# Kernel optimization log

Measured on AMD Instinct MI355X. Metric: run time of the kernel, lower is better.

## Reference

```python
import jax, jax.numpy as jnp
import numpy as np

HIDDEN = 512

def flip_sequences(x, lengths):
    # flax sst2-style flip: reverse each sequence's first `length` items, padding stays at end
    B, T = x.shape[0], x.shape[1]
    idxs = (jnp.arange(T - 1, -1, -1)[None, :] + lengths[:, None]) % T  # [B,T]
    return x[jnp.arange(B)[:, None], idxs]

def lstm_scan(x, Wi, Wh, b):
    # x: [B,T,D] -> outputs [B,T,H]; flax OptimizedLSTMCell math (gate order i,f,g,o)
    B = x.shape[0]
    H = Wh.shape[0]
    xW = jnp.einsum('btd,dg->tbg', x, Wi) + b  # precompute input projections, time-major [T,B,4H]
    def step(carry, xw):
        c, h = carry
        gates = xw + h @ Wh
        i, f, g, o = jnp.split(gates, 4, axis=-1)
        c = jax.nn.sigmoid(f) * c + jax.nn.sigmoid(i) * jnp.tanh(g)
        h = jax.nn.sigmoid(o) * jnp.tanh(c)
        return (c, h), h
    init = (jnp.zeros((B, H), x.dtype), jnp.zeros((B, H), x.dtype))
    _, hs = jax.lax.scan(step, init, xW)  # hs: [T,B,H]
    return jnp.swapaxes(hs, 0, 1)

def setup_inputs() -> dict:
    key = jax.random.key(0)
    ks = jax.random.split(key, 8)
    B, T, D, H = 16, 2048, 512, HIDDEN
    s_in = 1.0 / np.sqrt(D)
    s_h = 1.0 / np.sqrt(H)
    return {
        'inputs': jax.random.normal(ks[0], (B, T, D), jnp.float32),
        'lengths': jax.random.randint(ks[1], (B,), 1, T + 1, jnp.int32),
        'Wi_f': jax.random.normal(ks[2], (D, 4 * H), jnp.float32) * s_in,
        'Wh_f': jax.random.normal(ks[3], (H, 4 * H), jnp.float32) * s_h,
        'b_f': jnp.zeros((4 * H,), jnp.float32),
        'Wi_b': jax.random.normal(ks[4], (D, 4 * H), jnp.float32) * s_in,
        'Wh_b': jax.random.normal(ks[5], (H, 4 * H), jnp.float32) * s_h,
        'b_b': jnp.zeros((4 * H,), jnp.float32),
    }

def reference(inputs, lengths, Wi_f, Wh_f, b_f, Wi_b, Wh_b, b_b):
    fwd = lstm_scan(inputs, Wi_f, Wh_f, b_f)  # [B,T,H]
    rev_in = flip_sequences(inputs, lengths)
    bwd = lstm_scan(rev_in, Wi_b, Wh_b, b_b)
    bwd = flip_sequences(bwd, lengths)
    return jnp.concatenate([fwd, bwd], axis=-1)  # [B,T,2H]
```

## Files before the change

### kernel.cpp

```cpp
#include <hip/hip_runtime.h>
#include <cstdint>
#include <cstddef>

#define T_SEQ 2048
#define BATCH 16
#define DIM   512
#define HID   512
#define KTOT  1024
#define NCOL  2048
#define APAD  8
#define AROW  (KTOT + APAD)

typedef __attribute__((ext_vector_type(8))) short          s8v;
typedef __attribute__((ext_vector_type(4))) float          f4v;
typedef __attribute__((ext_vector_type(4))) unsigned short h4v;

__device__ __forceinline__ unsigned short f2b(float f) {
  unsigned u = __builtin_bit_cast(unsigned, f);
  return (unsigned short)((u + 0x7fffu + ((u >> 16) & 1u)) >> 16);
}

__global__ __launch_bounds__(256, 1)
void lstm_persist(const float* __restrict__ x, const int* __restrict__ lengths,
                  const float* __restrict__ Wi_f, const float* __restrict__ Wh_f,
                  const float* __restrict__ b_f,
                  const float* __restrict__ Wi_b, const float* __restrict__ Wh_b,
                  const float* __restrict__ b_b,
                  unsigned int* __restrict__ flags,
                  float* __restrict__ out) {
  __shared__ unsigned short A[BATCH][AROW];
  __shared__ float glds[4][BATCH][16];

  const int w    = (int)blockIdx.x;
  const int dir  = w >> 5;
  const int g    = w & 31;
  const int j0   = g * 16;
  const int tid  = (int)threadIdx.x;
  const int lane = tid & 63;
  const int wv   = tid >> 6;
  const int b    = tid >> 4;
  const int sub  = tid & 15;
  const int len  = lengths[b];

  const float* bias = dir ? b_b : b_f;
  const float bi = bias[0 * HID + j0 + sub];
  const float bf = bias[1 * HID + j0 + sub];
  const float bg = bias[2 * HID + j0 + sub];
  const float bo = bias[3 * HID + j0 + sub];

  s8v wfrag[32];
  {
    const float* Wi = dir ? Wi_b : Wi_f;
    const float* Wh = dir ? Wh_b : Wh_f;
    const int col = wv * HID + j0 + (lane & 15);
    const int kb  = (lane >> 4) * 8;
#pragma unroll
    for (int kc = 0; kc < 16; ++kc) {
      const float* src = Wi + (size_t)(kc * 32 + kb) * NCOL + col;
      s8v f;
#pragma unroll
      for (int j = 0; j < 8; ++j) f[j] = (short)f2b(src[(size_t)j * NCOL]);
      wfrag[kc] = f;
    }
#pragma unroll
    for (int kc = 0; kc < 16; ++kc) {
      const float* src = Wh + (size_t)(kc * 32 + kb) * NCOL + col;
      s8v f;
#pragma unroll
      for (int j = 0; j < 8; ++j) f[j] = (short)f2b(src[(size_t)j * NCOL]);
      wfrag[16 + kc] = f;
    }
  }

  float c_state = 0.f;
  const int arow = lane & 15;
  const int koff = (lane >> 4) * 8;
  unsigned int* myflag = flags + (size_t)(dir * 32 + g) * 16;
  unsigned int* pollbase = flags + (size_t)(dir * 32) * 16;

  {
    const int tau0 = dir ? ((T_SEQ - 1 + len) & (T_SEQ - 1)) : 0;
    const float* xrow = x + ((size_t)b * T_SEQ + tau0) * DIM;
#pragma unroll
    for (int r = 0; r < 8; ++r) {
      const int k = sub * 4 + r * 64;
      f4v v = *(const f4v*)(xrow + k);
      h4v p; p[0] = f2b(v[0]); p[1] = f2b(v[1]); p[2] = f2b(v[2]); p[3] = f2b(v[3]);
      *(h4v*)&A[b][k] = p;
      h4v z = (h4v){0, 0, 0, 0};
      *(h4v*)&A[b][DIM + k] = z;
    }
  }
  __syncthreads();

  for (int t = 0; t < T_SEQ; ++t) {
    const int tau = dir ? ((T_SEQ - 1 - t + len) & (T_SEQ - 1)) : t;
    const bool notlast = (t + 1 < T_SEQ);

    f4v xv[8];
    if (notlast) {
      const int taun = dir ? ((T_SEQ - 2 - t + len) & (T_SEQ - 1)) : (t + 1);
      const float* xrow = x + ((size_t)b * T_SEQ + taun) * DIM;
#pragma unroll
      for (int r = 0; r < 8; ++r) xv[r] = *(const f4v*)(xrow + sub * 4 + r * 64);
    }

    f4v acc0 = {0.f,0.f,0.f,0.f}, acc1 = {0.f,0.f,0.f,0.f};
    f4v acc2 = {0.f,0.f,0.f,0.f}, acc3 = {0.f,0.f,0.f,0.f};
    {
      const unsigned short* ap = &A[arow][koff];
#pragma unroll
      for (int kc = 0; kc < 32; kc += 4) {
        s8v a0 = *(const s8v*)(ap + (kc + 0) * 32);
        s8v a1 = *(const s8v*)(ap + (kc + 1) * 32);
        s8v a2 = *(const s8v*)(ap + (kc + 2) * 32);
        s8v a3 = *(const s8v*)(ap + (kc + 3) * 32);
        acc0 = __builtin_amdgcn_mfma_f32_16x16x32_bf16(a0, wfrag[kc + 0], acc0, 0, 0, 0);
        acc1 = __builtin_amdgcn_mfma_f32_16x16x32_bf16(a1, wfrag[kc + 1], acc1, 0, 0, 0);
        acc2 = __builtin_amdgcn_mfma_f32_16x16x32_bf16(a2, wfrag[kc + 2], acc2, 0, 0, 0);
        acc3 = __builtin_amdgcn_mfma_f32_16x16x32_bf16(a3, wfrag[kc + 3], acc3, 0, 0, 0);
      }
    }
#pragma unroll
    for (int r = 0; r < 4; ++r)
      glds[wv][(lane >> 4) * 4 + r][lane & 15] = (acc0[r] + acc1[r]) + (acc2[r] + acc3[r]);
    __syncthreads();

    {
      const float gi = glds[0][b][sub] + bi;
      const float gf = glds[1][b][sub] + bf;
      const float gg = glds[2][b][sub] + bg;
      const float go = glds[3][b][sub] + bo;
      const float si = 1.f / (1.f + __expf(-gi));
      const float sf = 1.f / (1.f + __expf(-gf));
      const float so = 1.f / (1.f + __expf(-go));
      const float tg = 1.f - 2.f / (1.f + __expf(2.f * gg));
      c_state = sf * c_state + si * tg;
      const float tc = 1.f - 2.f / (1.f + __expf(2.f * c_state));
      const float h = so * tc;
      __hip_atomic_store(out + ((size_t)b * T_SEQ + tau) * (2 * HID) + (size_t)dir * HID + j0 + sub,
                         h, __ATOMIC_RELAXED, __HIP_MEMORY_SCOPE_AGENT);
    }

    if (notlast) {
#pragma unroll
      for (int r = 0; r < 8; ++r) {
        const int k = sub * 4 + r * 64;
        h4v p; p[0] = f2b(xv[r][0]); p[1] = f2b(xv[r][1]);
               p[2] = f2b(xv[r][2]); p[3] = f2b(xv[r][3]);
        *(h4v*)&A[b][k] = p;
      }

      asm volatile("s_waitcnt vmcnt(0)" ::: "memory");
      __syncthreads();
      if (tid == 0)
        __hip_atomic_store(myflag, (unsigned)(t + 1), __ATOMIC_RELAXED, __HIP_MEMORY_SCOPE_AGENT);
      {
        const unsigned tgt = (unsigned)(t + 1);
        while (true) {
          unsigned v = __hip_atomic_load(pollbase + (size_t)(lane & 31) * 16,
                                         __ATOMIC_RELAXED, __HIP_MEMORY_SCOPE_AGENT);
          if (__all(v >= tgt)) break;
          __builtin_amdgcn_s_sleep(1);
        }
      }

      const float* hrow = out + ((size_t)b * T_SEQ + tau) * (2 * HID) + (size_t)dir * HID;
      unsigned long long hu[16];
#pragma unroll
      for (int r = 0; r < 8; ++r) {
        const int k = sub * 4 + r * 64;
        hu[2 * r]     = __hip_atomic_load((const unsigned long long*)(hrow + k),
                                          __ATOMIC_RELAXED, __HIP_MEMORY_SCOPE_AGENT);
        hu[2 * r + 1] = __hip_atomic_load((const unsigned long long*)(hrow + k) + 1,
                                          __ATOMIC_RELAXED, __HIP_MEMORY_SCOPE_AGENT);
      }
#pragma unroll
      for (int r = 0; r < 8; ++r) {
        const int k = sub * 4 + r * 64;
        const float f0 = __builtin_bit_cast(float, (unsigned)(hu[2 * r] & 0xffffffffu));
        const float f1 = __builtin_bit_cast(float, (unsigned)(hu[2 * r] >> 32));
        const float f2 = __builtin_bit_cast(float, (unsigned)(hu[2 * r + 1] & 0xffffffffu));
        const float f3 = __builtin_bit_cast(float, (unsigned)(hu[2 * r + 1] >> 32));
        h4v p; p[0] = f2b(f0); p[1] = f2b(f1); p[2] = f2b(f2); p[3] = f2b(f3);
        *(h4v*)&A[b][DIM + k] = p;
      }
      __syncthreads();
    }
  }
}

extern "C" void kernel_launch(void* const* d_in, const int* in_sizes, int n_in,
                              void* d_out, int out_size, void* d_ws, size_t ws_size,
                              hipStream_t stream) {
  const float* x    = (const float*)d_in[0];
  const int*   len  = (const int*)d_in[1];
  const float* Wi_f = (const float*)d_in[2];
  const float* Wh_f = (const float*)d_in[3];
  const float* b_f  = (const float*)d_in[4];
  const float* Wi_b = (const float*)d_in[5];
  const float* Wh_b = (const float*)d_in[6];
  const float* b_b  = (const float*)d_in[7];
  float* out = (float*)d_out;
  unsigned int* flags = (unsigned int*)d_ws;

  hipMemsetAsync(d_ws, 0, 4096, stream);
  hipLaunchKernelGGL(lstm_persist, dim3(64), dim3(256), 0, stream,
                     x, len, Wi_f, Wh_f, b_f, Wi_b, Wh_b, b_b, flags, out);
}
```

Before: 6.430 ms.

## Replace flag barrier with step-tagged bf16 hidden-state exchange buffer

```diff
diff --git a/kernel.cpp b/kernel.cpp
--- a/kernel.cpp
+++ b/kernel.cpp
@@ -15,6 +15,8 @@
 typedef __attribute__((ext_vector_type(4))) float          f4v;
 typedef __attribute__((ext_vector_type(4))) unsigned short h4v;
 
+#define HXIDX(d, s, b, j) (((((d) * 2 + (s)) * BATCH + (b)) * HID) + (j))
+
 __device__ __forceinline__ unsigned short f2b(float f) {
   unsigned u = __builtin_bit_cast(unsigned, f);
   return (unsigned short)((u + 0x7fffu + ((u >> 16) & 1u)) >> 16);
@@ -26,7 +28,7 @@
                   const float* __restrict__ b_f,
                   const float* __restrict__ Wi_b, const float* __restrict__ Wh_b,
                   const float* __restrict__ b_b,
-                  unsigned int* __restrict__ flags,
+                  unsigned int* __restrict__ hx,
                   float* __restrict__ out) {
   __shared__ unsigned short A[BATCH][AROW];
   __shared__ float glds[4][BATCH][16];
@@ -75,8 +77,6 @@
   float c_state = 0.f;
   const int arow = lane & 15;
   const int koff = (lane >> 4) * 8;
-  unsigned int* myflag = flags + (size_t)(dir * 32 + g) * 16;
-  unsigned int* pollbase = flags + (size_t)(dir * 32) * 16;
 
   {
     const int tau0 = dir ? ((T_SEQ - 1 + len) & (T_SEQ - 1)) : 0;
@@ -96,6 +96,7 @@
   for (int t = 0; t < T_SEQ; ++t) {
     const int tau = dir ? ((T_SEQ - 1 - t + len) & (T_SEQ - 1)) : t;
     const bool notlast = (t + 1 < T_SEQ);
+    const unsigned e = (unsigned)(t + 1);
 
     f4v xv[8];
     if (notlast) {
@@ -138,8 +139,12 @@
       c_state = sf * c_state + si * tg;
       const float tc = 1.f - 2.f / (1.f + __expf(2.f * c_state));
       const float h = so * tc;
-      __hip_atomic_store(out + ((size_t)b * T_SEQ + tau) * (2 * HID) + (size_t)dir * HID + j0 + sub,
-                         h, __ATOMIC_RELAXED, __HIP_MEMORY_SCOPE_AGENT);
+      if (notlast) {
+        const unsigned tagged = ((unsigned)f2b(h) << 16) | e;
+        __hip_atomic_store(&hx[HXIDX(dir, e & 1, b, j0 + sub)], tagged,
+                           __ATOMIC_RELAXED, __HIP_MEMORY_SCOPE_AGENT);
+      }
+      out[((size_t)b * T_SEQ + tau) * (2 * HID) + (size_t)dir * HID + j0 + sub] = h;
     }
 
     if (notlast) {
@@ -151,38 +156,32 @@
         *(h4v*)&A[b][k] = p;
       }
 
-      asm volatile("s_waitcnt vmcnt(0)" ::: "memory");
-      __syncthreads();
-      if (tid == 0)
-        __hip_atomic_store(myflag, (unsigned)(t + 1), __ATOMIC_RELAXED, __HIP_MEMORY_SCOPE_AGENT);
-      {
-        const unsigned tgt = (unsigned)(t + 1);
-        while (true) {
-          unsigned v = __hip_atomic_load(pollbase + (size_t)(lane & 31) * 16,
-                                         __ATOMIC_RELAXED, __HIP_MEMORY_SCOPE_AGENT);
-          if (__all(v >= tgt)) break;
-          __builtin_amdgcn_s_sleep(1);
+      const unsigned* hrow = hx + HXIDX(dir, e & 1, b, 0);
+      const unsigned long long msk = 0x0000FFFF0000FFFFULL;
+      const unsigned long long pat = ((unsigned long long)e << 32) | e;
+      unsigned long long hu[16];
+      while (true) {
+        bool ok = true;
+#pragma unroll
+        for (int r = 0; r < 8; ++r) {
+          const int k = sub * 4 + r * 64;
+          hu[2 * r]     = __hip_atomic_load((const unsigned long long*)(hrow + k),
+                                            __ATOMIC_RELAXED, __HIP_MEMORY_SCOPE_AGENT);
+          hu[2 * r + 1] = __hip_atomic_load((const unsigned long long*)(hrow + k) + 1,
+                                            __ATOMIC_RELAXED, __HIP_MEMORY_SCOPE_AGENT);
+          ok &= ((hu[2 * r] & msk) == pat) & ((hu[2 * r + 1] & msk) == pat);
         }
-      }
-
-      const float* hrow = out + ((size_t)b * T_SEQ + tau) * (2 * HID) + (size_t)dir * HID;
-      unsigned long long hu[16];
+        if (ok) break;
+        __builtin_amdgcn_s_sleep(1);
+      }
 #pragma unroll
       for (int r = 0; r < 8; ++r) {
         const int k = sub * 4 + r * 64;
-        hu[2 * r]     = __hip_atomic_load((const unsigned long long*)(hrow + k),
-                                          __ATOMIC_RELAXED, __HIP_MEMORY_SCOPE_AGENT);
-        hu[2 * r + 1] = __hip_atomic_load((const unsigned long long*)(hrow + k) + 1,
-                                          __ATOMIC_RELAXED, __HIP_MEMORY_SCOPE_AGENT);
-      }
-#pragma unroll
-      for (int r = 0; r < 8; ++r) {
-        const int k = sub * 4 + r * 64;
-        const float f0 = __builtin_bit_cast(float, (unsigned)(hu[2 * r] & 0xffffffffu));
-        const float f1 = __builtin_bit_cast(float, (unsigned)(hu[2 * r] >> 32));
-        const float f2 = __builtin_bit_cast(float, (unsigned)(hu[2 * r + 1] & 0xffffffffu));
-        const float f3 = __builtin_bit_cast(float, (unsigned)(hu[2 * r + 1] >> 32));
-        h4v p; p[0] = f2b(f0); p[1] = f2b(f1); p[2] = f2b(f2); p[3] = f2b(f3);
+        h4v p;
+        p[0] = (unsigned short)(hu[2 * r] >> 16);
+        p[1] = (unsigned short)(hu[2 * r] >> 48);
+        p[2] = (unsigned short)(hu[2 * r + 1] >> 16);
+        p[3] = (unsigned short)(hu[2 * r + 1] >> 48);
         *(h4v*)&A[b][DIM + k] = p;
       }
       __syncthreads();
@@ -202,9 +201,9 @@
   const float* Wh_b = (const float*)d_in[6];
   const float* b_b  = (const float*)d_in[7];
   float* out = (float*)d_out;
-  unsigned int* flags = (unsigned int*)d_ws;
-
-  hipMemsetAsync(d_ws, 0, 4096, stream);
+  unsigned int* hx = (unsigned int*)d_ws;
+
+  hipMemsetAsync(d_ws, 0, (size_t)2 * 2 * BATCH * HID * 4, stream);
   hipLaunchKernelGGL(lstm_persist, dim3(64), dim3(256), 0, stream,
-                     x, len, Wi_f, Wh_f, b_f, Wi_b, Wh_b, b_b, flags, out);
+                     x, len, Wi_f, Wh_f, b_f, Wi_b, Wh_b, b_b, hx, out);
 }
```

New measurement: 5.722 ms. 11.0% less time.
